# Kernel optimization log

Measured on AMD Instinct MI355X. Metric: run time of the kernel, lower is better.

Reference implementation:

```python
import jax, jax.numpy as jnp
import numpy as np

D = 1024
H = 16
DH = D // H
FF = 4096
EPS = 1e-6


def setup_inputs() -> dict:
    key = jax.random.key(0)
    ks = jax.random.split(key, 8)
    s = 1.0 / np.sqrt(D)
    return {
        "x": jax.random.normal(ks[0], (2, 2048, D), jnp.float32),
        # attention projections stored [in, out] (math equals torch Linear x @ W.T)
        "w_q": jax.random.normal(ks[1], (D, D), jnp.float32) * s,
        "w_k": jax.random.normal(ks[2], (D, D), jnp.float32) * s,
        "w_v": jax.random.normal(ks[3], (D, D), jnp.float32) * s,
        "w_o": jax.random.normal(ks[4], (D, D), jnp.float32) * s,
        "w1": jax.random.normal(ks[5], (D, FF), jnp.float32) * s,
        "b1": jnp.zeros((FF,), jnp.float32),
        "w2": jax.random.normal(ks[6], (FF, D), jnp.float32) * (1.0 / np.sqrt(FF)),
        "b2": jnp.zeros((D,), jnp.float32),
        "g1": jnp.ones((D,), jnp.float32),
        "be1": jnp.zeros((D,), jnp.float32),
        "g2": jnp.ones((D,), jnp.float32),
        "be2": jnp.zeros((D,), jnp.float32),
    }


def _layernorm(x, gamma, beta):
    # torch .std() uses Bessel correction (ddof=1); note std+eps, not var+eps
    mean = jnp.mean(x, axis=-1, keepdims=True)
    std = jnp.std(x, axis=-1, keepdims=True, ddof=1)
    return gamma * (x - mean) / (std + EPS) + beta


def _attention(h, w_q, w_k, w_v, w_o):
    B, S, _ = h.shape
    q = (h @ w_q).reshape(B, S, H, DH)
    k = (h @ w_k).reshape(B, S, H, DH)
    v = (h @ w_v).reshape(B, S, H, DH)
    scores = jnp.einsum('bqhd,bkhd->bhqk', q, k) / np.sqrt(DH)  # [B,H,S,S]
    attn = jax.nn.softmax(scores, axis=-1)
    out = jnp.einsum('bhqk,bkhd->bqhd', attn, v).reshape(B, S, D)
    return out @ w_o


def reference(x, w_q, w_k, w_v, w_o, w1, b1, w2, b2, g1, be1, g2, be2):
    # pre-norm residual 1: self-attention (dropout=0 / eval)
    x = x + _attention(_layernorm(x, g1, be1), w_q, w_k, w_v, w_o)
    # pre-norm residual 2: FFN
    h = _layernorm(x, g2, be2)
    x = x + (jax.nn.relu(h @ w1 + b1) @ w2 + b2)
    return x
```

## Files before the change

kernel.cpp:

```cpp
#include <hip/hip_runtime.h>


typedef _Float16 half8 __attribute__((ext_vector_type(8)));
typedef _Float16 half4 __attribute__((ext_vector_type(4)));
typedef __fp16 fp16x2 __attribute__((ext_vector_type(2)));
typedef float floatx4 __attribute__((ext_vector_type(4)));

#define MAX3(a, b, c) fmaxf(fmaxf((a), (b)), (c))

__device__ __forceinline__ void async16(const void* g, void* l) {
    __builtin_amdgcn_global_load_lds((const __attribute__((address_space(1))) unsigned int*)g,
                                     (__attribute__((address_space(3))) unsigned int*)l,
                                     16, 0, 0);
}

__global__ __launch_bounds__(256) void ln_kernel(const float* __restrict__ x,
                                                 const float* __restrict__ g,
                                                 const float* __restrict__ be,
                                                 _Float16* __restrict__ out) {
    int row = blockIdx.x;
    int tid = threadIdx.x;
    floatx4 v = ((const floatx4*)(x + (size_t)row * 1024))[tid];
    float s = 0.f, ss = 0.f;
#pragma unroll
    for (int i = 0; i < 4; i++) { s += v[i]; ss += v[i] * v[i]; }
#pragma unroll
    for (int off = 1; off < 64; off <<= 1) {
        s += __shfl_xor(s, off);
        ss += __shfl_xor(ss, off);
    }
    __shared__ float sm[8];
    int wave = tid >> 6, lane = tid & 63;
    if (lane == 0) { sm[wave] = s; sm[wave + 4] = ss; }
    __syncthreads();
    s = sm[0] + sm[1] + sm[2] + sm[3];
    ss = sm[4] + sm[5] + sm[6] + sm[7];
    float mean = s * (1.f / 1024.f);
    float var = (ss - s * mean) * (1.f / 1023.f);
    float rs = 1.f / (sqrtf(fmaxf(var, 0.f)) + 1e-6f);
    floatx4 gv = ((const floatx4*)g)[tid];
    floatx4 bv = ((const floatx4*)be)[tid];
    half4 o;
#pragma unroll
    for (int i = 0; i < 4; i++) o[i] = (_Float16)(gv[i] * (v[i] - mean) * rs + bv[i]);
    ((half4*)(out + (size_t)row * 1024))[tid] = o;
}

__device__ __forceinline__ void convt_body(const float* __restrict__ W, int ldW,
                                           _Float16* __restrict__ WT, int Kr, float scale,
                                           int n0, int k0) {
    __shared__ float t[64][65];
    int tid = threadIdx.x;
    int r = tid >> 4, c4 = (tid & 15) * 4;
#pragma unroll
    for (int p = 0; p < 4; p++) {
        floatx4 v = *(const floatx4*)(W + (size_t)(k0 + r + p * 16) * ldW + n0 + c4);
#pragma unroll
        for (int j = 0; j < 4; j++) t[c4 + j][r + p * 16] = v[j];
    }
    __syncthreads();
#pragma unroll
    for (int p = 0; p < 4; p++) {
        int rr = r + p * 16;
        half4 o;
#pragma unroll
        for (int j = 0; j < 4; j++) o[j] = (_Float16)(t[rr][c4 + j] * scale);
        *(half4*)(WT + (size_t)(n0 + rr) * Kr + k0 + c4) = o;
    }
}

__global__ __launch_bounds__(256) void convt_kernel(const float* __restrict__ W, int ldW,
                                                    _Float16* __restrict__ WT, int Kr,
                                                    float scale) {
    convt_body(W, ldW, WT, Kr, scale, blockIdx.x * 64, blockIdx.y * 64);
}

__global__ __launch_bounds__(256) void convt3_kernel(const float* __restrict__ W0,
                                                     const float* __restrict__ W1,
                                                     const float* __restrict__ W2,
                                                     _Float16* __restrict__ QT) {
    int z = blockIdx.z;
    const float* W = (z == 0) ? W0 : (z == 1) ? W1 : W2;
    _Float16* WT = QT + (size_t)z * 1024 * 1024;
    float scale = (z == 0) ? 0.125f : 1.f;
    convt_body(W, 1024, WT, 1024, scale, blockIdx.x * 64, blockIdx.y * 64);
}

__global__ __launch_bounds__(256) void convt_pair_kernel(const float* __restrict__ Wa, int ldWa,
                                                         _Float16* __restrict__ WTa, int Kra,
                                                         int gxa, int gya,
                                                         const float* __restrict__ Wb, int ldWb,
                                                         _Float16* __restrict__ WTb, int Krb,
                                                         int gxb, int gyb) {
    int z = blockIdx.z;
    const float* W = z ? Wb : Wa;
    _Float16* WT = z ? WTb : WTa;
    int ldW = z ? ldWb : ldWa;
    int Kr = z ? Krb : Kra;
    int gx = z ? gxb : gxa, gy = z ? gyb : gya;
    if ((int)blockIdx.x >= gx || (int)blockIdx.y >= gy) return;
    convt_body(W, ldW, WT, Kr, 1.f, blockIdx.x * 64, blockIdx.y * 64);
}

__global__ __launch_bounds__(256) void transv_kernel(const _Float16* __restrict__ V, int ldv,
                                                     _Float16* __restrict__ Vt) {
    __shared__ _Float16 t[64][72];
    int t0 = blockIdx.x * 64, d0 = blockIdx.y * 64;
    int tid = threadIdx.x;
#pragma unroll
    for (int i = 0; i < 2; i++) {
        int v = tid + i * 256;
        int r = v >> 3, c = (v & 7) * 8;
        half8 vv = *(const half8*)(V + (size_t)(t0 + r) * ldv + d0 + c);
#pragma unroll
        for (int j = 0; j < 8; j++) t[c + j][r] = vv[j];
    }
    __syncthreads();
    int bh = (t0 >> 11) * 16 + (d0 >> 6);
    int sbase = t0 & 2047;
#pragma unroll
    for (int i = 0; i < 2; i++) {
        int v = tid + i * 256;
        int r = v >> 3, c = (v & 7) * 8;
        half8 o = *(const half8*)&t[r][c];
        *(half8*)(Vt + ((size_t)bh * 64 + r) * 2048 + sbase + c) = o;
    }
}

__global__ __launch_bounds__(256) void gemm_t(const _Float16* __restrict__ A, int lda,
                                              const _Float16* __restrict__ BT,
                                              const float* __restrict__ bias,
                                              const float* res, void* Cout,
                                              int N, int K, int relu_flag, int out_fp16) {
    __shared__ _Float16 As[64 * 64];
    __shared__ _Float16 Bs[128 * 64];
    int tid = threadIdx.x;
    int wave = tid >> 6, lane = tid & 63, quad = lane >> 4, l15 = lane & 15;
    int bm = blockIdx.y * 64, bn = blockIdx.x * 128;
    int wr = (wave & 1) * 32, wc = (wave >> 1) * 64;
    int lrow = lane >> 3, lch = lane & 7;

    floatx4 acc[2][4];
#pragma unroll
    for (int im = 0; im < 2; im++)
#pragma unroll
        for (int in = 0; in < 4; in++)
#pragma unroll
            for (int r = 0; r < 4; r++) acc[im][in][r] = 0.f;

    for (int k0 = 0; k0 < K; k0 += 64) {
        __syncthreads();
#pragma unroll
        for (int ia = 0; ia < 2; ia++) {
            int g = 2 * wave + ia;
            int row = g * 8 + lrow;
            int ch = lch ^ (row & 7);
            async16(A + (size_t)(bm + row) * lda + k0 + ch * 8, &As[g * 512]);
        }
#pragma unroll
        for (int ib = 0; ib < 4; ib++) {
            int g = 4 * wave + ib;
            int row = g * 8 + lrow;
            int ch = lch ^ (row & 7);
            async16(BT + (size_t)(bn + row) * K + k0 + ch * 8, &Bs[g * 512]);
        }
        __syncthreads();

        half8 af[2][2], bf[4][2];
#pragma unroll
        for (int kk = 0; kk < 2; kk++) {
#pragma unroll
            for (int im = 0; im < 2; im++) {
                int m = wr + im * 16 + l15;
                af[im][kk] = *(const half8*)&As[m * 64 + ((((kk << 2) | quad) ^ (m & 7)) << 3)];
            }
#pragma unroll
            for (int in = 0; in < 4; in++) {
                int n = wc + in * 16 + l15;
                bf[in][kk] = *(const half8*)&Bs[n * 64 + ((((kk << 2) | quad) ^ (n & 7)) << 3)];
            }
        }
#pragma unroll
        for (int kk = 0; kk < 2; kk++)
#pragma unroll
            for (int im = 0; im < 2; im++)
#pragma unroll
                for (int in = 0; in < 4; in++)
                    acc[im][in] = __builtin_amdgcn_mfma_f32_16x16x32_f16(af[im][kk], bf[in][kk],
                                                                         acc[im][in], 0, 0, 0);
    }
#pragma unroll
    for (int im = 0; im < 2; im++)
#pragma unroll
        for (int in = 0; in < 4; in++)
#pragma unroll
            for (int r = 0; r < 4; r++) {
                int row = bm + wr + im * 16 + quad * 4 + r;
                int col = bn + wc + in * 16 + l15;
                float val = acc[im][in][r];
                if (bias) val += bias[col];
                if (relu_flag) val = fmaxf(val, 0.f);
                if (res) val += res[(size_t)row * N + col];
                if (out_fp16) ((_Float16*)Cout)[(size_t)row * N + col] = (_Float16)val;
                else          ((float*)Cout)[(size_t)row * N + col] = val;
            }
}

__global__ __launch_bounds__(256) void gemm_t128(const _Float16* __restrict__ A, int lda,
                                                 const _Float16* __restrict__ BT,
                                                 const float* __restrict__ bias,
                                                 const float* res, void* Cout,
                                                 int N, int K, int relu_flag, int out_fp16) {
    __shared__ _Float16 As[128 * 64];
    __shared__ _Float16 Bs[128 * 64];
    int tid = threadIdx.x;
    int wave = tid >> 6, lane = tid & 63, quad = lane >> 4, l15 = lane & 15;
    int bm = blockIdx.y * 128, bn = blockIdx.x * 128;
    int wr = (wave & 1) * 64, wc = (wave >> 1) * 64;
    int lrow = lane >> 3, lch = lane & 7;

    floatx4 acc[4][4];
#pragma unroll
    for (int im = 0; im < 4; im++)
#pragma unroll
        for (int in = 0; in < 4; in++)
#pragma unroll
            for (int r = 0; r < 4; r++) acc[im][in][r] = 0.f;

    for (int k0 = 0; k0 < K; k0 += 64) {
        __syncthreads();
#pragma unroll
        for (int ia = 0; ia < 4; ia++) {
            int g = 4 * wave + ia;
            int row = g * 8 + lrow;
            int ch = lch ^ (row & 7);
            async16(A + (size_t)(bm + row) * lda + k0 + ch * 8, &As[g * 512]);
        }
#pragma unroll
        for (int ib = 0; ib < 4; ib++) {
            int g = 4 * wave + ib;
            int row = g * 8 + lrow;
            int ch = lch ^ (row & 7);
            async16(BT + (size_t)(bn + row) * K + k0 + ch * 8, &Bs[g * 512]);
        }
        __syncthreads();

        half8 af[4][2], bf[4][2];
#pragma unroll
        for (int kk = 0; kk < 2; kk++) {
#pragma unroll
            for (int im = 0; im < 4; im++) {
                int m = wr + im * 16 + l15;
                af[im][kk] = *(const half8*)&As[m * 64 + ((((kk << 2) | quad) ^ (m & 7)) << 3)];
            }
#pragma unroll
            for (int in = 0; in < 4; in++) {
                int n = wc + in * 16 + l15;
                bf[in][kk] = *(const half8*)&Bs[n * 64 + ((((kk << 2) | quad) ^ (n & 7)) << 3)];
            }
        }
#pragma unroll
        for (int kk = 0; kk < 2; kk++)
#pragma unroll
            for (int im = 0; im < 4; im++)
#pragma unroll
                for (int in = 0; in < 4; in++)
                    acc[im][in] = __builtin_amdgcn_mfma_f32_16x16x32_f16(af[im][kk], bf[in][kk],
                                                                         acc[im][in], 0, 0, 0);
    }
#pragma unroll
    for (int im = 0; im < 4; im++)
#pragma unroll
        for (int in = 0; in < 4; in++)
#pragma unroll
            for (int r = 0; r < 4; r++) {
                int row = bm + wr + im * 16 + quad * 4 + r;
                int col = bn + wc + in * 16 + l15;
                float val = acc[im][in][r];
                if (bias) val += bias[col];
                if (relu_flag) val = fmaxf(val, 0.f);
                if (res) val += res[(size_t)row * N + col];
                if (out_fp16) ((_Float16*)Cout)[(size_t)row * N + col] = (_Float16)val;
                else          ((float*)Cout)[(size_t)row * N + col] = val;
            }
}

template <int BUF>
__device__ __forceinline__ void attn_step(const half8* const (&kfp)[2][4][2],
                                          const half4* const (&vfp)[2][4][4],
                                          const half8 (&bq)[2],
                                          floatx4 (&o_acc)[4],
                                          float& m_i, float& l_i) {
    const float LOG2E = 1.44269504f;
    floatx4 s_acc[4];
#pragma unroll
    for (int jn = 0; jn < 4; jn++)
#pragma unroll
        for (int r = 0; r < 4; r++) s_acc[jn][r] = 0.f;
#pragma unroll
    for (int jn = 0; jn < 4; jn++)
#pragma unroll
        for (int kk = 0; kk < 2; kk++)
            s_acc[jn] = __builtin_amdgcn_mfma_f32_16x16x32_f16(*kfp[BUF][jn][kk], bq[kk],
                                                               s_acc[jn], 0, 0, 0);

    float t0 = MAX3(s_acc[0][0], s_acc[0][1], s_acc[0][2]);
    float t1 = MAX3(s_acc[0][3], s_acc[1][0], s_acc[1][1]);
    float t2 = MAX3(s_acc[1][2], s_acc[1][3], s_acc[2][0]);
    float t3 = MAX3(s_acc[2][1], s_acc[2][2], s_acc[2][3]);
    float t4 = MAX3(s_acc[3][0], s_acc[3][1], s_acc[3][2]);
    float mx = MAX3(MAX3(t0, t1, t2), fmaxf(t3, t4), s_acc[3][3]);
    mx = fmaxf(mx, __shfl_xor(mx, 16));
    mx = fmaxf(mx, __shfl_xor(mx, 32));
    if (!__all(mx <= m_i + 8.f)) {
        float mnew = fmaxf(m_i, mx);
        float dd = m_i - mnew;
        float alpha = (dd < -60.f) ? 0.f : __expf(dd);
        l_i *= alpha;
#pragma unroll
        for (int im = 0; im < 4; im++)
#pragma unroll
            for (int r = 0; r < 4; r++) o_acc[im][r] *= alpha;
        m_i = mnew;
    }
    float m2 = m_i * LOG2E;

    float sj[4];
    half4 pb[4];
#pragma unroll
    for (int jn = 0; jn < 4; jn++) {
        float p0 = exp2f(fmaf(s_acc[jn][0], LOG2E, -m2));
        float p1 = exp2f(fmaf(s_acc[jn][1], LOG2E, -m2));
        float p2 = exp2f(fmaf(s_acc[jn][2], LOG2E, -m2));
        float p3 = exp2f(fmaf(s_acc[jn][3], LOG2E, -m2));
        sj[jn] = (p0 + p1) + (p2 + p3);
        fp16x2 lo = __builtin_amdgcn_cvt_pkrtz(p0, p1);
        fp16x2 hi = __builtin_amdgcn_cvt_pkrtz(p2, p3);
        pb[jn][0] = (_Float16)lo[0]; pb[jn][1] = (_Float16)lo[1];
        pb[jn][2] = (_Float16)hi[0]; pb[jn][3] = (_Float16)hi[1];
    }
    float sum = (sj[0] + sj[1]) + (sj[2] + sj[3]);
    sum += __shfl_xor(sum, 16);
    sum += __shfl_xor(sum, 32);
    l_i += sum;

#pragma unroll
    for (int im = 0; im < 4; im++)
#pragma unroll
        for (int ks = 0; ks < 4; ks++)
            o_acc[im] = __builtin_amdgcn_mfma_f32_16x16x16f16(*vfp[BUF][im][ks], pb[ks],
                                                              o_acc[im], 0, 0, 0);
}

__global__ __launch_bounds__(256) void attn_kernel(const _Float16* Q,
                                                   const _Float16* __restrict__ K,
                                                   const _Float16* __restrict__ Vt,
                                                   _Float16* O, int ld) {
    __shared__ _Float16 KVs[2][2][64 * 64];
    int qt = blockIdx.x, bh = blockIdx.y;
    int b = bh >> 4, h = bh & 15;
    int col0 = h * 64, tbase = b * 2048;
    int tid = threadIdx.x;
    int wave = tid >> 6, lane = tid & 63, quad = lane >> 4, l15 = lane & 15;
    int lrow = lane >> 3, lch = lane & 7;

    const _Float16* kg[2];
    const _Float16* vg[2];
    const size_t kadv = (size_t)64 * ld;
#pragma unroll
    for (int i = 0; i < 2; i++) {
        int g = 2 * wave + i;
        int row = g * 8 + lrow;
        int ch = lch ^ (row & 7);
        kg[i] = K + (size_t)(tbase + row) * ld + col0 + ch * 8;
        vg[i] = Vt + ((size_t)bh * 64 + row) * 2048 + ch * 8;
        async16(Q + (size_t)(tbase + qt * 64 + row) * ld + col0 + ch * 8, &KVs[1][0][g * 512]);
        async16(kg[i], &KVs[0][0][g * 512]);
        async16(vg[i], &KVs[0][1][g * 512]);
        kg[i] += kadv;
        vg[i] += 64;
    }
    __syncthreads();

    int rowq = 16 * wave + l15;
    half8 bq[2];
#pragma unroll
    for (int kk = 0; kk < 2; kk++)
        bq[kk] = *(const half8*)&KVs[1][0][rowq * 64 + ((((kk << 2) | quad) ^ (rowq & 7)) << 3)];
    asm volatile("s_waitcnt lgkmcnt(0)" ::: "memory");
    __builtin_amdgcn_sched_barrier(0);

    const half8* kfp[2][4][2];
    const half4* vfp[2][4][4];
#pragma unroll
    for (int bb = 0; bb < 2; bb++) {
#pragma unroll
        for (int jn = 0; jn < 4; jn++) {
            int rowk = 16 * jn + l15;
#pragma unroll
            for (int kk = 0; kk < 2; kk++)
                kfp[bb][jn][kk] = (const half8*)
                    &KVs[bb][0][rowk * 64 + ((((kk << 2) | quad) ^ (rowk & 7)) << 3)];
        }
#pragma unroll
        for (int im = 0; im < 4; im++) {
            int rowv = 16 * im + l15;
#pragma unroll
            for (int ks = 0; ks < 4; ks++) {
                int off = rowv * 128 + ((((2 * ks) | (quad >> 1)) ^ (rowv & 7)) << 4)
                          + (quad & 1) * 8;
                vfp[bb][im][ks] = (const half4*)((const char*)KVs[bb][1] + off);
            }
        }
    }

    floatx4 o_acc[4];
#pragma unroll
    for (int im = 0; im < 4; im++)
#pragma unroll
        for (int r = 0; r < 4; r++) o_acc[im][r] = 0.f;
    float m_i = -1e30f, l_i = 0.f;

#pragma unroll 1
    for (int kt2 = 0; kt2 < 16; kt2++) {
        if (kt2) __syncthreads();
#pragma unroll
        for (int i = 0; i < 2; i++) {
            async16(kg[i], &KVs[1][0][(2 * wave + i) * 512]);
            async16(vg[i], &KVs[1][1][(2 * wave + i) * 512]);
            kg[i] += kadv;
            vg[i] += 64;
        }
        attn_step<0>(kfp, vfp, bq, o_acc, m_i, l_i);

        __syncthreads();
        if (kt2 < 15) {
#pragma unroll
            for (int i = 0; i < 2; i++) {
                async16(kg[i], &KVs[0][0][(2 * wave + i) * 512]);
                async16(vg[i], &KVs[0][1][(2 * wave + i) * 512]);
                kg[i] += kadv;
                vg[i] += 64;
            }
        }
        attn_step<1>(kfp, vfp, bq, o_acc, m_i, l_i);
    }

    float rl = 1.f / l_i;
#pragma unroll
    for (int im = 0; im < 4; im++) {
        half4 o;
#pragma unroll
        for (int r = 0; r < 4; r++) o[r] = (_Float16)(o_acc[im][r] * rl);
        *(half4*)&O[(size_t)(tbase + qt * 64 + wave * 16 + l15) * ld + col0 + im * 16 + quad * 4] = o;
    }
}

extern "C" void kernel_launch(void* const* d_in, const int* in_sizes, int n_in,
                              void* d_out, int out_size, void* d_ws, size_t ws_size,
                              hipStream_t stream) {
    const float* x   = (const float*)d_in[0];
    const float* wq  = (const float*)d_in[1];
    const float* wk  = (const float*)d_in[2];
    const float* wv  = (const float*)d_in[3];
    const float* wo  = (const float*)d_in[4];
    const float* w1  = (const float*)d_in[5];
    const float* b1  = (const float*)d_in[6];
    const float* w2  = (const float*)d_in[7];
    const float* b2  = (const float*)d_in[8];
    const float* g1  = (const float*)d_in[9];
    const float* be1 = (const float*)d_in[10];
    const float* g2  = (const float*)d_in[11];
    const float* be2 = (const float*)d_in[12];

    const size_t M1 = (size_t)1 << 20;
    _Float16* R0  = (_Float16*)d_ws;
    _Float16* QKV = R0 + 4 * M1;
    _Float16* R3  = R0 + 12 * M1;

    _Float16* wqkvT = (_Float16*)d_out;
    float* x1 = (float*)d_out;
    float* out = (float*)d_out;

    dim3 blk(256);

    convt3_kernel<<<dim3(16, 16, 3), blk, 0, stream>>>(wq, wk, wv, wqkvT);
    ln_kernel<<<4096, blk, 0, stream>>>(x, g1, be1, R0);
    gemm_t128<<<dim3(24, 32), blk, 0, stream>>>(R0, 1024, wqkvT, nullptr, nullptr, QKV, 3072, 1024, 0, 1);
    transv_kernel<<<dim3(64, 16), blk, 0, stream>>>(QKV + 2048, 3072, R0);
    attn_kernel<<<dim3(32, 32), blk, 0, stream>>>(QKV, QKV + 1024, R0, QKV, 3072);
    _Float16* woT = R0;
    convt_kernel<<<dim3(16, 16), blk, 0, stream>>>(wo, 1024, woT, 1024, 1.f);
    gemm_t<<<dim3(8, 64), blk, 0, stream>>>(QKV, 3072, woT, nullptr, x, x1, 1024, 1024, 0, 0);
    ln_kernel<<<4096, blk, 0, stream>>>(x1, g2, be2, R0);
    _Float16* f = QKV;
    for (int hh = 0; hh < 2; hh++) {
        _Float16* w1Th = R3;
        _Float16* w2Th = R3 + 2 * M1;
        convt_pair_kernel<<<dim3(32, 32, 2), blk, 0, stream>>>(
            w1 + hh * 2048, 4096, w1Th, 1024, 32, 16,
            w2 + (size_t)hh * 2048 * 1024, 1024, w2Th, 2048, 16, 32);
        gemm_t128<<<dim3(16, 32), blk, 0, stream>>>(R0, 1024, w1Th, b1 + hh * 2048, nullptr, f,
                                                    2048, 1024, 1, 1);
        gemm_t<<<dim3(8, 64), blk, 0, stream>>>(f, 2048, w2Th, (hh == 1) ? b2 : nullptr, x1, out,
                                                1024, 2048, 0, 0);
    }
}
```

Measured before the change: 450.3 us.

## Add double-buffered 64x128 GEMM for N=1024 projections and retile FFN1

Adds a gemm_t_db kernel with two LDS buffers for the 64x128 tile, so the async global-to-LDS load of the next K slice overlaps the MFMA work on the current one. It is used for the output projection and the FFN down projection. FFN1 switches from the 128x128 kernel to the 64x128 gemm_t with a larger grid, and the attention P packing uses a bitcast instead of per-element moves. Double buffering doubles LDS use per block, which may lower occupancy, and the loop assumes K/64 is even.

```diff
diff --git a/kernel.cpp b/kernel.cpp
--- a/kernel.cpp
+++ b/kernel.cpp
@@ -4,6 +4,7 @@
 typedef _Float16 half8 __attribute__((ext_vector_type(8)));
 typedef _Float16 half4 __attribute__((ext_vector_type(4)));
 typedef __fp16 fp16x2 __attribute__((ext_vector_type(2)));
+typedef unsigned int uintx2 __attribute__((ext_vector_type(2)));
 typedef float floatx4 __attribute__((ext_vector_type(4)));
 
 #define MAX3(a, b, c) fmaxf(fmaxf((a), (b)), (c))
@@ -206,6 +207,97 @@
             }
 }
 
+__global__ __launch_bounds__(256) void gemm_t_db(const _Float16* __restrict__ A, int lda,
+                                                 const _Float16* __restrict__ BT,
+                                                 const float* __restrict__ bias,
+                                                 const float* res, void* Cout,
+                                                 int N, int K, int relu_flag, int out_fp16) {
+    __shared__ _Float16 As[2][64 * 64];
+    __shared__ _Float16 Bs[2][128 * 64];
+    int tid = threadIdx.x;
+    int wave = tid >> 6, lane = tid & 63, quad = lane >> 4, l15 = lane & 15;
+    int bm = blockIdx.y * 64, bn = blockIdx.x * 128;
+    int wr = (wave & 1) * 32, wc = (wave >> 1) * 64;
+    int lrow = lane >> 3, lch = lane & 7;
+
+    floatx4 acc[2][4];
+#pragma unroll
+    for (int im = 0; im < 2; im++)
+#pragma unroll
+        for (int in = 0; in < 4; in++)
+#pragma unroll
+            for (int r = 0; r < 4; r++) acc[im][in][r] = 0.f;
+
+    auto stage = [&](int buf, int k0) {
+#pragma unroll
+        for (int ia = 0; ia < 2; ia++) {
+            int g = 2 * wave + ia;
+            int row = g * 8 + lrow;
+            int ch = lch ^ (row & 7);
+            async16(A + (size_t)(bm + row) * lda + k0 + ch * 8, &As[buf][g * 512]);
+        }
+#pragma unroll
+        for (int ib = 0; ib < 4; ib++) {
+            int g = 4 * wave + ib;
+            int row = g * 8 + lrow;
+            int ch = lch ^ (row & 7);
+            async16(BT + (size_t)(bn + row) * K + k0 + ch * 8, &Bs[buf][g * 512]);
+        }
+    };
+    auto compute = [&](int buf) {
+        half8 af[2][2], bf[4][2];
+#pragma unroll
+        for (int kk = 0; kk < 2; kk++) {
+#pragma unroll
+            for (int im = 0; im < 2; im++) {
+                int m = wr + im * 16 + l15;
+                af[im][kk] = *(const half8*)&As[buf][m * 64 + ((((kk << 2) | quad) ^ (m & 7)) << 3)];
+            }
+#pragma unroll
+            for (int in = 0; in < 4; in++) {
+                int n = wc + in * 16 + l15;
+                bf[in][kk] = *(const half8*)&Bs[buf][n * 64 + ((((kk << 2) | quad) ^ (n & 7)) << 3)];
+            }
+        }
+#pragma unroll
+        for (int kk = 0; kk < 2; kk++)
+#pragma unroll
+            for (int im = 0; im < 2; im++)
+#pragma unroll
+                for (int in = 0; in < 4; in++)
+                    acc[im][in] = __builtin_amdgcn_mfma_f32_16x16x32_f16(af[im][kk], bf[in][kk],
+                                                                         acc[im][in], 0, 0, 0);
+    };
+
+    int nk = K >> 6;
+    stage(0, 0);
+#pragma unroll 1
+    for (int t2 = 0; t2 < (nk >> 1); t2++) {
+        int ke = t2 << 1;
+        __syncthreads();
+        if (ke + 1 < nk) stage(1, (ke + 1) << 6);
+        compute(0);
+        __syncthreads();
+        if (ke + 2 < nk) stage(0, (ke + 2) << 6);
+        compute(1);
+    }
+#pragma unroll
+    for (int im = 0; im < 2; im++)
+#pragma unroll
+        for (int in = 0; in < 4; in++)
+#pragma unroll
+            for (int r = 0; r < 4; r++) {
+                int row = bm + wr + im * 16 + quad * 4 + r;
+                int col = bn + wc + in * 16 + l15;
+                float val = acc[im][in][r];
+                if (bias) val += bias[col];
+                if (relu_flag) val = fmaxf(val, 0.f);
+                if (res) val += res[(size_t)row * N + col];
+                if (out_fp16) ((_Float16*)Cout)[(size_t)row * N + col] = (_Float16)val;
+                else          ((float*)Cout)[(size_t)row * N + col] = val;
+            }
+}
+
 __global__ __launch_bounds__(256) void gemm_t128(const _Float16* __restrict__ A, int lda,
                                                  const _Float16* __restrict__ BT,
                                                  const float* __restrict__ bias,
@@ -336,8 +428,10 @@
         sj[jn] = (p0 + p1) + (p2 + p3);
         fp16x2 lo = __builtin_amdgcn_cvt_pkrtz(p0, p1);
         fp16x2 hi = __builtin_amdgcn_cvt_pkrtz(p2, p3);
-        pb[jn][0] = (_Float16)lo[0]; pb[jn][1] = (_Float16)lo[1];
-        pb[jn][2] = (_Float16)hi[0]; pb[jn][3] = (_Float16)hi[1];
+        uintx2 both;
+        both[0] = __builtin_bit_cast(unsigned int, lo);
+        both[1] = __builtin_bit_cast(unsigned int, hi);
+        pb[jn] = __builtin_bit_cast(half4, both);
     }
     float sum = (sj[0] + sj[1]) + (sj[2] + sj[3]);
     sum += __shfl_xor(sum, 16);
@@ -491,7 +585,7 @@
     attn_kernel<<<dim3(32, 32), blk, 0, stream>>>(QKV, QKV + 1024, R0, QKV, 3072);
     _Float16* woT = R0;
     convt_kernel<<<dim3(16, 16), blk, 0, stream>>>(wo, 1024, woT, 1024, 1.f);
-    gemm_t<<<dim3(8, 64), blk, 0, stream>>>(QKV, 3072, woT, nullptr, x, x1, 1024, 1024, 0, 0);
+    gemm_t_db<<<dim3(8, 64), blk, 0, stream>>>(QKV, 3072, woT, nullptr, x, x1, 1024, 1024, 0, 0);
     ln_kernel<<<4096, blk, 0, stream>>>(x1, g2, be2, R0);
     _Float16* f = QKV;
     for (int hh = 0; hh < 2; hh++) {
@@ -500,9 +594,9 @@
         convt_pair_kernel<<<dim3(32, 32, 2), blk, 0, stream>>>(
             w1 + hh * 2048, 4096, w1Th, 1024, 32, 16,
             w2 + (size_t)hh * 2048 * 1024, 1024, w2Th, 2048, 16, 32);
-        gemm_t128<<<dim3(16, 32), blk, 0, stream>>>(R0, 1024, w1Th, b1 + hh * 2048, nullptr, f,
-                                                    2048, 1024, 1, 1);
-        gemm_t<<<dim3(8, 64), blk, 0, stream>>>(f, 2048, w2Th, (hh == 1) ? b2 : nullptr, x1, out,
-                                                1024, 2048, 0, 0);
-    }
-}
+        gemm_t<<<dim3(16, 64), blk, 0, stream>>>(R0, 1024, w1Th, b1 + hh * 2048, nullptr, f,
+                                                 2048, 1024, 1, 1);
+        gemm_t_db<<<dim3(8, 64), blk, 0, stream>>>(f, 2048, w2Th, (hh == 1) ? b2 : nullptr, x1, out,
+                                                   1024, 2048, 0, 0);
+    }
+}
```

Result: no change. 454.1 us (+0.8%).
